# Optimization experiments

Measured on AMD Instinct MI355X. Metric: run time of the kernel, lower is better.

The kernel has to match this reference:

```python
import jax, jax.numpy as jnp
import numpy as np

N = 4096          # number of agents
TOP_K = 12        # config.TOP_K
OBS_RADIUS = 1.0  # config.OBS_RADIUS


def setup_inputs() -> dict:
    key = jax.random.key(0)
    ks = jax.random.split(key, 10)

    def lin(k, o, i):
        return jax.random.normal(k, (o, i), dtype=jnp.float32) * (1.0 / np.sqrt(i))

    x = jax.random.normal(ks[0], (N, N, 4), dtype=jnp.float32)
    r = jnp.asarray(0.25, dtype=jnp.float32)  # safety radius subtracted from d_norm
    W1 = lin(ks[1], 64, 6);   b1 = jax.random.normal(ks[2], (64,), jnp.float32) * 0.01
    W2 = lin(ks[3], 128, 64); b2 = jax.random.normal(ks[4], (128,), jnp.float32) * 0.01
    W3 = lin(ks[5], 64, 128); b3 = jax.random.normal(ks[6], (64,), jnp.float32) * 0.01
    W4 = lin(ks[7], 1, 64);   b4 = jax.random.normal(ks[8], (1,), jnp.float32) * 0.01
    return {"x": x, "r": r, "W1": W1, "b1": b1, "W2": W2, "b2": b2,
            "W3": W3, "b3": b3, "W4": W4, "b4": b4}


def reference(x, r, W1, b1, W2, b2, W3, b3, W4, b4):
    n = x.shape[0]
    # d_norm with eps added INSIDE the sum (matches torch: sum(x**2 + 1e-4))
    d_norm = jnp.sqrt(jnp.sum(x[:, :, :2] ** 2 + 0.0001, axis=2, keepdims=True))  # [n,n,1]
    eye = jnp.eye(n, dtype=x.dtype)[:, :, None]                                   # [n,n,1]
    xf = jnp.concatenate([x, eye, d_norm - r], axis=2)                            # [n,n,6]

    # remove_distant_agents: top-k nearest by 2D norm (eps 1e-6 inside sum)
    dn = jnp.sqrt(jnp.sum(xf[:, :, :2] ** 2 + 1e-06, axis=2))                     # [n,n]
    _, idx = jax.lax.top_k(-dn, TOP_K)                                            # [n,K]
    xg = jnp.take_along_axis(xf, idx[:, :, None], axis=1)                         # [n,K,6]

    dist = jnp.sqrt(jnp.sum(xg[:, :, :2] ** 2 + 0.0001, axis=2, keepdims=True))   # [n,K,1]
    mask = (dist <= OBS_RADIUS).astype(xg.dtype)

    # 1x1 Conv1d stack == per-neighbor MLP
    h = jax.nn.relu(jnp.einsum('nkc,oc->nko', xg, W1) + b1)
    h = jax.nn.relu(jnp.einsum('nkc,oc->nko', h, W2) + b2)
    h = jax.nn.relu(jnp.einsum('nkc,oc->nko', h, W3) + b3)
    out = (jnp.einsum('nkc,oc->nko', h, W4) + b4) * mask                          # [n,K,1]

    rows = jnp.broadcast_to(jnp.arange(n)[:, None], (n, TOP_K))
    indices = jnp.stack([rows, idx], axis=2).reshape(-1, 2)                       # [n*K,2]
    return out, mask, indices
```

## Files before the change

kernel.cpp:

```cpp
#include <hip/hip_runtime.h>

#define NN    4096
#define TOPK  12
#define NP    (NN * TOPK)
#define OFF_MASK (NP)
#define OFF_IDX  (2 * NP)

__global__ __launch_bounds__(256, 6) void topk_rows(const float* __restrict__ x,
                                                    float* __restrict__ out) {
    const int i    = blockIdx.x;
    const int t    = threadIdx.x;
    const int lane = t & 63;
    const int w    = t >> 6;
    const float4* x4 = (const float4*)x + (size_t)i * NN;

    float s[16];
    #pragma unroll
    for (int k = 0; k < 16; ++k) {
        float4 v = x4[(k << 8) + t];
        s[k] = v.x * v.x + v.y * v.y;
    }

    unsigned long long bk;
    {
        float bs = s[0]; int bj = t;
        #pragma unroll
        for (int k = 1; k < 16; ++k) {
            int j = (k << 8) + t;
            if (s[k] < bs) { bs = s[k]; bj = j; }
        }
        bk = ((unsigned long long)__float_as_uint(bs) << 32) | (unsigned)bj;
    }

    __shared__ unsigned long long cand[4 * TOPK];

    unsigned long long mykey = ~0ULL;

    for (int it = 0; it < TOPK; ++it) {
        unsigned long long vk = bk;
        #pragma unroll
        for (int off = 1; off < 64; off <<= 1) {
            unsigned long long ok = __shfl_xor(vk, off, 64);
            vk = (ok < vk) ? ok : vk;
        }
        if (lane == it) mykey = vk;
        int wj = (int)(vk & 0xffffffffULL);
        if ((wj & 63) == lane) {
            int kk = wj >> 8;
            #pragma unroll
            for (int k = 0; k < 16; ++k)
                if (k == kk) s[k] = 3.0e38f;
            float bs = s[0]; int bj = t;
            #pragma unroll
            for (int k = 1; k < 16; ++k) {
                int j = (k << 8) + t;
                if (s[k] < bs) { bs = s[k]; bj = j; }
            }
            bk = ((unsigned long long)__float_as_uint(bs) << 32) | (unsigned)bj;
        }
    }

    if (lane < TOPK) cand[w * TOPK + lane] = mykey;
    __syncthreads();

    if (w == 0) {
        unsigned long long key = (lane < 4 * TOPK) ? cand[lane] : ~0ULL;
        #pragma unroll
        for (int k = 2; k <= 64; k <<= 1) {
            #pragma unroll
            for (int jj = k >> 1; jj >= 1; jj >>= 1) {
                unsigned long long ok = __shfl_xor(key, jj, 64);
                bool keepMin = ((lane & k) == 0) == ((lane & jj) == 0);
                unsigned long long mn = (ok < key) ? ok : key;
                unsigned long long mx = (ok < key) ? key : ok;
                key = keepMin ? mn : mx;
            }
        }
        if (lane < TOPK) {
            int   j  = (int)(key & 0xffffffffULL);
            float ss = __uint_as_float((unsigned)(key >> 32));
            float d  = sqrtf(ss + 2.0e-4f);
            float mask = (d <= 1.0f) ? 1.0f : 0.0f;
            int p = i * TOPK + lane;
            out[OFF_MASK + p]        = mask;
            out[OFF_IDX + 2 * p]     = (float)i;
            out[OFF_IDX + 2 * p + 1] = (float)j;
        }
    }
}

__global__ __launch_bounds__(512, 6) void mlp_block(
        const float* __restrict__ x, const float* __restrict__ rp,
        const float* __restrict__ W1, const float* __restrict__ b1,
        const float* __restrict__ W2, const float* __restrict__ b2,
        const float* __restrict__ W3, const float* __restrict__ b3,
        const float* __restrict__ W4, const float* __restrict__ b4,
        float* out) {
    __shared__ float h1s[64 * 64];
    __shared__ float h2s[128 * 64];
    __shared__ float p4s[8 * 64];

    const int t  = threadIdx.x;
    const int pl = t & 63;
    const int ch = __builtin_amdgcn_readfirstlane(t >> 6);
    const int p  = blockIdx.x * 64 + pl;
    const int i  = p / TOPK;
    const int j  = (int)out[OFF_IDX + 2 * p + 1];

    const float4 v = ((const float4*)x)[(size_t)i * NN + j];
    const float d  = sqrtf(v.x * v.x + v.y * v.y + 2.0e-4f);
    float xin[6];
    xin[0] = v.x; xin[1] = v.y; xin[2] = v.z; xin[3] = v.w;
    xin[4] = (i == j) ? 1.0f : 0.0f;
    xin[5] = d - rp[0];

    #pragma unroll
    for (int q = 0; q < 8; ++q) {
        int m = ch * 8 + q;
        const float* w = W1 + m * 6;
        float a = b1[m];
        #pragma unroll
        for (int c = 0; c < 6; ++c) a += w[c] * xin[c];
        h1s[m * 64 + pl] = fmaxf(a, 0.0f);
    }
    __syncthreads();

    float acc[16];
    #pragma unroll
    for (int q = 0; q < 16; ++q) acc[q] = b2[ch * 16 + q];
    for (int part = 0; part < 4; ++part) {
        float h1r[16];
        #pragma unroll
        for (int k = 0; k < 16; ++k) h1r[k] = h1s[(part * 16 + k) * 64 + pl];
        #pragma unroll
        for (int q = 0; q < 16; ++q) {
            const float* w = W2 + (ch * 16 + q) * 64 + part * 16;
            #pragma unroll
            for (int k = 0; k < 16; ++k) acc[q] += w[k] * h1r[k];
        }
    }
    #pragma unroll
    for (int q = 0; q < 16; ++q) h2s[(ch * 16 + q) * 64 + pl] = fmaxf(acc[q], 0.0f);
    __syncthreads();

    float h3[8];
    #pragma unroll
    for (int q = 0; q < 8; ++q) h3[q] = b3[ch * 8 + q];
    for (int part = 0; part < 8; ++part) {
        float h2r[16];
        #pragma unroll
        for (int k = 0; k < 16; ++k) h2r[k] = h2s[(part * 16 + k) * 64 + pl];
        #pragma unroll
        for (int q = 0; q < 8; ++q) {
            const float* w = W3 + (ch * 8 + q) * 128 + part * 16;
            #pragma unroll
            for (int k = 0; k < 16; ++k) h3[q] += w[k] * h2r[k];
        }
    }
    float partial = 0.0f;
    #pragma unroll
    for (int q = 0; q < 8; ++q) partial += W4[ch * 8 + q] * fmaxf(h3[q], 0.0f);
    p4s[ch * 64 + pl] = partial;
    __syncthreads();

    if (t < 64) {
        float s = b4[0];
        #pragma unroll
        for (int c = 0; c < 8; ++c) s += p4s[c * 64 + t];
        int pp = blockIdx.x * 64 + t;
        out[pp] = s * out[OFF_MASK + pp];
    }
}

extern "C" void kernel_launch(void* const* d_in, const int* in_sizes, int n_in,
                              void* d_out, int out_size, void* d_ws, size_t ws_size,
                              hipStream_t stream) {
    const float* x  = (const float*)d_in[0];
    const float* rp = (const float*)d_in[1];
    const float* W1 = (const float*)d_in[2];
    const float* b1 = (const float*)d_in[3];
    const float* W2 = (const float*)d_in[4];
    const float* b2 = (const float*)d_in[5];
    const float* W3 = (const float*)d_in[6];
    const float* b3 = (const float*)d_in[7];
    const float* W4 = (const float*)d_in[8];
    const float* b4 = (const float*)d_in[9];
    float* out = (float*)d_out;

    topk_rows<<<NN, 256, 0, stream>>>(x, out);
    mlp_block<<<NP / 64, 512, 0, stream>>>(x, rp, W1, b1, W2, b2, W3, b3, W4, b4, out);
}
```

Baseline: 411.2 us.

## Replace iterative top-k extraction with threshold-based candidate filtering

Measured after the change: 405.2 us, median of 3. Within noise of the previous version (-1.5%).

```diff
diff --git a/kernel.cpp b/kernel.cpp
--- a/kernel.cpp
+++ b/kernel.cpp
@@ -5,6 +5,21 @@
 #define NP    (NN * TOPK)
 #define OFF_MASK (NP)
 #define OFF_IDX  (2 * NP)
+
+__device__ __forceinline__ unsigned long long bitonic64(unsigned long long key, int lane) {
+    #pragma unroll
+    for (int k = 2; k <= 64; k <<= 1) {
+        #pragma unroll
+        for (int jj = k >> 1; jj >= 1; jj >>= 1) {
+            unsigned long long ok = __shfl_xor(key, jj, 64);
+            bool keepMin = ((lane & k) == 0) == ((lane & jj) == 0);
+            unsigned long long mn = (ok < key) ? ok : key;
+            unsigned long long mx = (ok < key) ? key : ok;
+            key = keepMin ? mn : mx;
+        }
+    }
+    return key;
+}
 
 __global__ __launch_bounds__(256, 6) void topk_rows(const float* __restrict__ x,
                                                     float* __restrict__ out) {
@@ -21,21 +36,79 @@
         s[k] = v.x * v.x + v.y * v.y;
     }
 
-    unsigned long long bk;
+    float bs = s[0]; int bj = t;
+    #pragma unroll
+    for (int k = 1; k < 16; ++k) {
+        int j = (k << 8) + t;
+        if (s[k] < bs) { bs = s[k]; bj = j; }
+    }
+    unsigned long long bk =
+        ((unsigned long long)__float_as_uint(bs) << 32) | (unsigned)bj;
+
+    __shared__ unsigned long long cand[64];
+    __shared__ unsigned long long wtop[4 * TOPK];
+    __shared__ float Tsh;
+    __shared__ int   cnt[4];
+
     {
-        float bs = s[0]; int bj = t;
-        #pragma unroll
-        for (int k = 1; k < 16; ++k) {
-            int j = (k << 8) + t;
-            if (s[k] < bs) { bs = s[k]; bj = j; }
-        }
-        bk = ((unsigned long long)__float_as_uint(bs) << 32) | (unsigned)bj;
-    }
-
-    __shared__ unsigned long long cand[4 * TOPK];
+        unsigned long long key = bitonic64(bk, lane);
+        if (lane < TOPK) wtop[w * TOPK + lane] = key;
+    }
+    __syncthreads();
+
+    if (w == 0) {
+        unsigned long long k2 = (lane < 4 * TOPK) ? wtop[lane] : ~0ULL;
+        k2 = bitonic64(k2, lane);
+        if (lane == TOPK - 1) Tsh = __uint_as_float((unsigned)(k2 >> 32));
+    }
+    __syncthreads();
+    const float T = Tsh;
+
+    int c = 0;
+    #pragma unroll
+    for (int k = 0; k < 16; ++k) c += (s[k] <= T) ? 1 : 0;
+
+    int pfx = c;
+    #pragma unroll
+    for (int off = 1; off < 64; off <<= 1) {
+        int o = __shfl_up(pfx, off, 64);
+        if (lane >= off) pfx += o;
+    }
+    if (lane == 63) cnt[w] = pfx;
+    __syncthreads();
+
+    const int total = cnt[0] + cnt[1] + cnt[2] + cnt[3];
+
+    if (total <= 64) {
+        int base = 0;
+        for (int ww = 0; ww < w; ++ww) base += cnt[ww];
+        int o = base + (pfx - c);
+        #pragma unroll
+        for (int k = 0; k < 16; ++k) {
+            if (s[k] <= T)
+                cand[o++] = ((unsigned long long)__float_as_uint(s[k]) << 32)
+                            | (unsigned)((k << 8) + t);
+        }
+        __syncthreads();
+
+        if (w == 0) {
+            unsigned long long k3 = (lane < total) ? cand[lane] : ~0ULL;
+            k3 = bitonic64(k3, lane);
+            if (lane < TOPK) {
+                int   j  = (int)(k3 & 0xffffffffULL);
+                float ss = __uint_as_float((unsigned)(k3 >> 32));
+                float d  = sqrtf(ss + 2.0e-4f);
+                float m  = (d <= 1.0f) ? 1.0f : 0.0f;
+                int p = i * TOPK + lane;
+                out[OFF_MASK + p]        = m;
+                out[OFF_IDX + 2 * p]     = (float)i;
+                out[OFF_IDX + 2 * p + 1] = (float)j;
+            }
+        }
+        return;
+    }
 
     unsigned long long mykey = ~0ULL;
-
     for (int it = 0; it < TOPK; ++it) {
         unsigned long long vk = bk;
         #pragma unroll
@@ -50,39 +123,28 @@
             #pragma unroll
             for (int k = 0; k < 16; ++k)
                 if (k == kk) s[k] = 3.0e38f;
-            float bs = s[0]; int bj = t;
+            float nbs = s[0]; int nbj = t;
             #pragma unroll
             for (int k = 1; k < 16; ++k) {
                 int j = (k << 8) + t;
-                if (s[k] < bs) { bs = s[k]; bj = j; }
+                if (s[k] < nbs) { nbs = s[k]; nbj = j; }
             }
-            bk = ((unsigned long long)__float_as_uint(bs) << 32) | (unsigned)bj;
-        }
-    }
-
+            bk = ((unsigned long long)__float_as_uint(nbs) << 32) | (unsigned)nbj;
+        }
+    }
     if (lane < TOPK) cand[w * TOPK + lane] = mykey;
     __syncthreads();
 
     if (w == 0) {
-        unsigned long long key = (lane < 4 * TOPK) ? cand[lane] : ~0ULL;
-        #pragma unroll
-        for (int k = 2; k <= 64; k <<= 1) {
-            #pragma unroll
-            for (int jj = k >> 1; jj >= 1; jj >>= 1) {
-                unsigned long long ok = __shfl_xor(key, jj, 64);
-                bool keepMin = ((lane & k) == 0) == ((lane & jj) == 0);
-                unsigned long long mn = (ok < key) ? ok : key;
-                unsigned long long mx = (ok < key) ? key : ok;
-                key = keepMin ? mn : mx;
-            }
-        }
+        unsigned long long k3 = (lane < 4 * TOPK) ? cand[lane] : ~0ULL;
+        k3 = bitonic64(k3, lane);
         if (lane < TOPK) {
-            int   j  = (int)(key & 0xffffffffULL);
-            float ss = __uint_as_float((unsigned)(key >> 32));
+            int   j  = (int)(k3 & 0xffffffffULL);
+            float ss = __uint_as_float((unsigned)(k3 >> 32));
             float d  = sqrtf(ss + 2.0e-4f);
-            float mask = (d <= 1.0f) ? 1.0f : 0.0f;
+            float m  = (d <= 1.0f) ? 1.0f : 0.0f;
             int p = i * TOPK + lane;
-            out[OFF_MASK + p]        = mask;
+            out[OFF_MASK + p]        = m;
             out[OFF_IDX + 2 * p]     = (float)i;
             out[OFF_IDX + 2 * p + 1] = (float)j;
         }
```
